# Kernel tuning notes

Hardware: AMD Instinct MI355X
Metric: run time of the kernel (lower is better)

## Reference

```python
import jax, jax.numpy as jnp
import numpy as np

B, L, D = 8, 1024, 512
H, DK, DV = 8, 64, 64
EPS = 1e-6
NEG = -1e9


def setup_inputs() -> dict:
    key = jax.random.key(0)
    ks = jax.random.split(key, 12)
    def xavier(k, shape):
        fan_out, fan_in = shape
        bound = float(np.sqrt(6.0 / (fan_in + fan_out)))
        return jax.random.uniform(k, shape, jnp.float32, -bound, bound)
    return {
        "q": jax.random.normal(ks[0], (B, L, D), jnp.float32),
        "k": jax.random.normal(ks[1], (B, L, D), jnp.float32),
        "v": jax.random.normal(ks[2], (B, L, D), jnp.float32),
        "event_type": jax.random.randint(ks[3], (B, L), 0, 2, jnp.int32),
        "mask": jax.random.randint(ks[4], (B, L, L), 0, 2, jnp.int32).astype(bool),
        "w_qs": xavier(ks[5], (H * DK, D)),
        "w_ex_en_qs": xavier(ks[6], (H * DK, D)),
        "w_ks": xavier(ks[7], (H * DK, D)),
        "w_vs": xavier(ks[8], (H * DV, D)),
        "w_fc": xavier(ks[9], (D, H * DV)),
        "b_fc": jnp.zeros((D,), jnp.float32),
        "ln_gamma": jnp.ones((D,), jnp.float32),
        "ln_beta": jnp.zeros((D,), jnp.float32),
    }


def _layer_norm(x, gamma, beta):
    mu = jnp.mean(x, axis=-1, keepdims=True)
    var = jnp.var(x, axis=-1, keepdims=True)
    return (x - mu) * jax.lax.rsqrt(var + EPS) * gamma + beta


def reference(q, k, v, event_type, mask, w_qs, w_ex_en_qs, w_ks, w_vs, w_fc, b_fc, ln_gamma, ln_beta):
    residual = q
    qn = _layer_norm(q, ln_gamma, ln_beta)  # normalize_before=True

    # event-type flags: en_en = prev is en AND present is en; ex_en = prev is ex AND present is en
    is_en = event_type != 0                                   # [B, L]
    en_en = (is_en[:, :, None] & is_en[:, None, :])[:, None]  # [B, 1, L, L]
    ex_en = ((~is_en)[:, :, None] & is_en[:, None, :])[:, None]

    def proj(x, w, d):  # torch Linear: x @ w.T, then split heads -> [B, H, L, d]
        return (x @ w.T).reshape(B, L, H, d).transpose(0, 2, 1, 3)

    q_en = proj(qn, w_qs, DK)
    q_ex = proj(qn, w_ex_en_qs, DK)
    kh = proj(k, w_ks, DK)
    vh = proj(v, w_vs, DV)

    temp = jnp.asarray(DK ** 0.5, qn.dtype)
    scores_en = jnp.einsum('bhqd,bhkd->bhqk', q_en / temp, kh)
    scores_en = jnp.where(mask[:, None], NEG, scores_en)      # masked branch
    scores_ex = jnp.einsum('bhqd,bhkd->bhqk', q_ex / temp, kh)  # unmasked branch

    blended = en_en * scores_en + ex_en * scores_ex           # [B, H, L, L]
    attn = jax.nn.softmax(blended, axis=-1)

    out = jnp.einsum('bhqk,bhkd->bhqd', attn, vh)             # PV
    out = out.transpose(0, 2, 1, 3).reshape(B, L, H * DV)
    out = out @ w_fc.T + b_fc
    out = out + residual
    return out, attn
```

## Files before the change

### kernel.cpp

```cpp
#include <hip/hip_runtime.h>

typedef __attribute__((ext_vector_type(8))) short bf16x8;
typedef __attribute__((ext_vector_type(4))) float f32x4;

#define DEVI static __device__ __forceinline__

constexpr float NEGV = -1e9f;

DEVI unsigned short f2b(float f) {
  union { float f; unsigned int u; } c; c.f = f;
  unsigned int lsb = (c.u >> 16) & 1u;
  return (unsigned short)((c.u + 0x7fffu + lsb) >> 16);
}
DEVI float sb2f(short s) {
  union { unsigned int u; float f; } c;
  c.u = ((unsigned int)(unsigned short)s) << 16;
  return c.f;
}

__global__ void mask_detect(const unsigned int* __restrict__ m, int n, int* flag) {
  unsigned int v = 0;
  for (int i = blockIdx.x * blockDim.x + threadIdx.x; i < n; i += gridDim.x * blockDim.x)
    v |= m[i];
  if (v & ~1u) atomicOr(flag, 1);
}

__global__ void mask_canon_bits(const void* __restrict__ mraw, unsigned int* __restrict__ mb,
                                int nwords, const int* __restrict__ flag) {
  int i = blockIdx.x * blockDim.x + threadIdx.x;
  if (i >= nwords) return;
  bool isbytes = (*flag != 0);
  unsigned int out = 0;
  if (isbytes) {
    const unsigned int* p = (const unsigned int*)mraw + (size_t)i * 8;
    #pragma unroll
    for (int w = 0; w < 8; w++) {
      unsigned int bw = p[w];
      out |= ((bw & 1u) << (w * 4)) | (((bw >> 8) & 1u) << (w * 4 + 1)) |
             (((bw >> 16) & 1u) << (w * 4 + 2)) | (((bw >> 24) & 1u) << (w * 4 + 3));
    }
  } else {
    const int4* p = (const int4*)mraw + (size_t)i * 8;
    #pragma unroll
    for (int w = 0; w < 8; w++) {
      int4 v = p[w];
      out |= ((v.x != 0 ? 1u : 0u) << (w * 4)) | ((v.y != 0 ? 1u : 0u) << (w * 4 + 1)) |
             ((v.z != 0 ? 1u : 0u) << (w * 4 + 2)) | ((v.w != 0 ? 1u : 0u) << (w * 4 + 3));
    }
  }
  mb[i] = out;
}

__global__ __launch_bounds__(256) void ln_kernel(const float* __restrict__ q,
    const float* __restrict__ gamma, const float* __restrict__ beta,
    unsigned short* __restrict__ qn) {
  int row = blockIdx.x;
  int t = threadIdx.x;
  const float* x = q + (size_t)row * 512;
  float2 v = reinterpret_cast<const float2*>(x)[t];
  float s = v.x + v.y, s2 = v.x * v.x + v.y * v.y;
  #pragma unroll
  for (int o = 32; o; o >>= 1) { s += __shfl_xor(s, o); s2 += __shfl_xor(s2, o); }
  __shared__ float ls[4], ls2[4];
  int w = t >> 6;
  if ((t & 63) == 0) { ls[w] = s; ls2[w] = s2; }
  __syncthreads();
  float S = ls[0] + ls[1] + ls[2] + ls[3];
  float S2 = ls2[0] + ls2[1] + ls2[2] + ls2[3];
  float mu = S * (1.f / 512.f);
  float var = S2 * (1.f / 512.f) - mu * mu;
  float r = rsqrtf(var + 1e-6f);
  float g0 = gamma[t * 2], g1 = gamma[t * 2 + 1];
  float b0 = beta[t * 2], b1 = beta[t * 2 + 1];
  ushort2 o;
  o.x = f2b((v.x - mu) * r * g0 + b0);
  o.y = f2b((v.y - mu) * r * g1 + b1);
  reinterpret_cast<ushort2*>(qn + (size_t)row * 512)[t] = o;
}

template<int MODE, bool CVX, bool CVW>
__global__ __launch_bounds__(256) void gemm_bt(
    const void* __restrict__ Xv,
    const void* __restrict__ Wv,
    void* __restrict__ Yv,
    float scale,
    const float* __restrict__ bias,
    const float* __restrict__ resid) {
  constexpr int LDT = 40;
  __shared__ __align__(16) unsigned short lA[64 * LDT];
  __shared__ __align__(16) unsigned short lB[64 * LDT];
  int t = threadIdx.x;
  int w = t >> 6, l = t & 63, lr = l & 15, lg = l >> 4;
  int mb = blockIdx.x * 64, nb = blockIdx.y * 64;
  f32x4 acc[4];
  #pragma unroll
  for (int n = 0; n < 4; n++) acc[n] = {0.f, 0.f, 0.f, 0.f};
  int sr = t >> 2, sc = (t & 3) * 8;
  for (int k0 = 0; k0 < 512; k0 += 32) {
    __syncthreads();
    if constexpr (CVX) {
      const float* src = (const float*)Xv + (size_t)(mb + sr) * 512 + k0 + sc;
      float4 x0 = *reinterpret_cast<const float4*>(src);
      float4 x1 = *reinterpret_cast<const float4*>(src + 4);
      ushort4 h0{f2b(x0.x), f2b(x0.y), f2b(x0.z), f2b(x0.w)};
      ushort4 h1{f2b(x1.x), f2b(x1.y), f2b(x1.z), f2b(x1.w)};
      *reinterpret_cast<ushort4*>(&lA[sr * LDT + sc]) = h0;
      *reinterpret_cast<ushort4*>(&lA[sr * LDT + sc + 4]) = h1;
    } else {
      *reinterpret_cast<float4*>(&lA[sr * LDT + sc]) =
          *reinterpret_cast<const float4*>((const unsigned short*)Xv + (size_t)(mb + sr) * 512 + k0 + sc);
    }
    if constexpr (CVW) {
      const float* src = (const float*)Wv + (size_t)(nb + sr) * 512 + k0 + sc;
      float4 x0 = *reinterpret_cast<const float4*>(src);
      float4 x1 = *reinterpret_cast<const float4*>(src + 4);
      ushort4 h0{f2b(x0.x), f2b(x0.y), f2b(x0.z), f2b(x0.w)};
      ushort4 h1{f2b(x1.x), f2b(x1.y), f2b(x1.z), f2b(x1.w)};
      *reinterpret_cast<ushort4*>(&lB[sr * LDT + sc]) = h0;
      *reinterpret_cast<ushort4*>(&lB[sr * LDT + sc + 4]) = h1;
    } else {
      *reinterpret_cast<float4*>(&lB[sr * LDT + sc]) =
          *reinterpret_cast<const float4*>((const unsigned short*)Wv + (size_t)(nb + sr) * 512 + k0 + sc);
    }
    __syncthreads();
    bf16x8 a = *reinterpret_cast<const bf16x8*>(&lA[(w * 16 + lr) * LDT + lg * 8]);
    #pragma unroll
    for (int n = 0; n < 4; n++) {
      bf16x8 bb = *reinterpret_cast<const bf16x8*>(&lB[(n * 16 + lr) * LDT + lg * 8]);
      acc[n] = __builtin_amdgcn_mfma_f32_16x16x32_bf16(a, bb, acc[n], 0, 0, 0);
    }
  }
  #pragma unroll
  for (int n = 0; n < 4; n++) {
    #pragma unroll
    for (int j = 0; j < 4; j++) {
      int m = mb + w * 16 + lg * 4 + j;
      int c = nb + n * 16 + lr;
      float val = acc[n][j] * scale;
      if constexpr (MODE == 0) {
        reinterpret_cast<unsigned short*>(Yv)[(size_t)m * 512 + c] = f2b(val);
      } else if constexpr (MODE == 1) {
        int bb_ = m >> 10, ll = m & 1023, hh = c >> 6, dd = c & 63;
        reinterpret_cast<unsigned short*>(Yv)[((size_t)((bb_ * 8 + hh) * 64 + dd)) * 1024 + ll] = f2b(val);
      } else {
        reinterpret_cast<float*>(Yv)[(size_t)m * 512 + c] =
            val + bias[c] + resid[(size_t)m * 512 + c];
      }
    }
  }
}

__global__ __launch_bounds__(256) void attn_kernel(
    const unsigned short* __restrict__ qen,
    const unsigned short* __restrict__ qex,
    const unsigned short* __restrict__ kh,
    const unsigned short* __restrict__ vhT,
    const int* __restrict__ etype,
    const unsigned int* __restrict__ mbits,
    float* __restrict__ attn_g,
    unsigned short* __restrict__ pv_out) {
  int lid = blockIdx.x;
  int xcd = lid & 7, slot = lid >> 3;
  int qt = slot & 15;
  int g = ((slot >> 4) << 3) | xcd;
  int h = g & 7, b = g >> 3;

  int t = threadIdx.x, w = t >> 6, l = t & 63, lr = l & 15, lg = l >> 4;
  __shared__ unsigned int ekbits[32];
  __shared__ unsigned int mkill[64 * 33];
  __shared__ __align__(16) unsigned short pbuf[4][16][40];

  int qb = qt * 64 + w * 16;
  int qrowA = qb + lr;
  bool evA = etype[b * 1024 + qrowA] != 0;
  const unsigned short* qp = evA ? qen : qex;
  size_t qoff = (size_t)(b * 1024 + qrowA) * 512 + h * 64;
  bf16x8 a0 = *reinterpret_cast<const bf16x8*>(qp + qoff + lg * 8);
  bf16x8 a1 = *reinterpret_cast<const bf16x8*>(qp + qoff + 32 + lg * 8);

  if (t < 32) {
    unsigned int wdd = 0;
    const int4* ep = (const int4*)(etype + b * 1024 + t * 32);
    #pragma unroll
    for (int j4 = 0; j4 < 8; j4++) {
      int4 e = ep[j4];
      wdd |= ((e.x != 0 ? 1u : 0u) << (j4 * 4)) | ((e.y != 0 ? 1u : 0u) << (j4 * 4 + 1)) |
             ((e.z != 0 ? 1u : 0u) << (j4 * 4 + 2)) | ((e.w != 0 ? 1u : 0u) << (j4 * 4 + 3));
    }
    ekbits[t] = wdd;
  }
  {
    const unsigned int* mslice = mbits + ((size_t)(b * 1024 + qt * 64)) * 32;
    for (int i = t; i < 2048; i += 256) {
      int row = i >> 5, wd = i & 31;
      bool evq_row = etype[b * 1024 + qt * 64 + row] != 0;
      mkill[row * 33 + wd] = evq_row ? mslice[i] : 0u;
    }
  }
  __syncthreads();

  int qrc[4], qlc[4];
  #pragma unroll
  for (int j = 0; j < 4; j++) { qlc[j] = w * 16 + lg * 4 + j; qrc[j] = qt * 64 + qlc[j]; }

  const unsigned short* kptr = kh + ((size_t)b * 1024 + lr) * 512 + h * 64 + lg * 8;
  const unsigned short* vptr = vhT + ((size_t)((b * 8 + h) * 64) + lr) * 1024 + lg * 8;

  float srun[4] = {0.f, 0.f, 0.f, 0.f};
  #pragma unroll 4
  for (int kt = 0; kt < 64; kt++) {
    const unsigned short* kp = kptr + (size_t)kt * 16 * 512;
    bf16x8 b0 = *reinterpret_cast<const bf16x8*>(kp);
    bf16x8 b1 = *reinterpret_cast<const bf16x8*>(kp + 32);
    f32x4 cc = {0.f, 0.f, 0.f, 0.f};
    cc = __builtin_amdgcn_mfma_f32_16x16x32_bf16(a0, b0, cc, 0, 0, 0);
    cc = __builtin_amdgcn_mfma_f32_16x16x32_bf16(a1, b1, cc, 0, 0, 0);
    int wcol = kt >> 1, bitpos = ((kt & 1) << 4) + lr;
    bool ekb = (ekbits[wcol] >> bitpos) & 1;
    #pragma unroll
    for (int j = 0; j < 4; j++) {
      bool mk = (mkill[qlc[j] * 33 + wcol] >> bitpos) & 1;
      float val = ekb ? (mk ? NEGV : cc[j]) : 0.f;
      srun[j] += __expf(val);
    }
  }
  float rS[4];
  #pragma unroll
  for (int j = 0; j < 4; j++) {
    float s = srun[j];
    s += __shfl_xor(s, 1); s += __shfl_xor(s, 2);
    s += __shfl_xor(s, 4); s += __shfl_xor(s, 8);
    rS[j] = 1.f / s;
  }

  f32x4 oacc[4];
  #pragma unroll
  for (int n = 0; n < 4; n++) oacc[n] = {0.f, 0.f, 0.f, 0.f};
  float* ag = attn_g + ((size_t)(b * 8 + h)) * 1024 * 1024;
  float* agrow = ag + (size_t)(qb + lr) * 1024 + lg * 8;

  #pragma unroll 2
  for (int kt = 0; kt < 64; kt++) {
    const unsigned short* kp = kptr + (size_t)kt * 16 * 512;
    bf16x8 b0 = *reinterpret_cast<const bf16x8*>(kp);
    bf16x8 b1 = *reinterpret_cast<const bf16x8*>(kp + 32);
    f32x4 cc = {0.f, 0.f, 0.f, 0.f};
    cc = __builtin_amdgcn_mfma_f32_16x16x32_bf16(a0, b0, cc, 0, 0, 0);
    cc = __builtin_amdgcn_mfma_f32_16x16x32_bf16(a1, b1, cc, 0, 0, 0);
    int wcol = kt >> 1, bitpos = ((kt & 1) << 4) + lr;
    bool ekb = (ekbits[wcol] >> bitpos) & 1;
    #pragma unroll
    for (int j = 0; j < 4; j++) {
      bool mk = (mkill[qlc[j] * 33 + wcol] >> bitpos) & 1;
      float val = ekb ? (mk ? NEGV : cc[j]) : 0.f;
      float p = __expf(val) * rS[j];
      pbuf[w][lg * 4 + j][((kt & 1) << 4) + lr] = f2b(p);
    }
    if (kt & 1) {
      int kc = kt >> 1;
      bf16x8 pa = *reinterpret_cast<const bf16x8*>(&pbuf[w][lr][lg * 8]);
      f32x4 f0, f1;
      f0[0] = sb2f(pa[0]); f0[1] = sb2f(pa[1]); f0[2] = sb2f(pa[2]); f0[3] = sb2f(pa[3]);
      f1[0] = sb2f(pa[4]); f1[1] = sb2f(pa[5]); f1[2] = sb2f(pa[6]); f1[3] = sb2f(pa[7]);
      __builtin_nontemporal_store(f0, reinterpret_cast<f32x4*>(agrow + kc * 32));
      __builtin_nontemporal_store(f1, reinterpret_cast<f32x4*>(agrow + kc * 32 + 4));
      #pragma unroll
      for (int n = 0; n < 4; n++) {
        const unsigned short* vp = vptr + (size_t)n * 16 * 1024 + kc * 32;
        bf16x8 vb = *reinterpret_cast<const bf16x8*>(vp);
        oacc[n] = __builtin_amdgcn_mfma_f32_16x16x32_bf16(pa, vb, oacc[n], 0, 0, 0);
      }
    }
  }
  #pragma unroll
  for (int n = 0; n < 4; n++) {
    #pragma unroll
    for (int j = 0; j < 4; j++) {
      __builtin_nontemporal_store(f2b(oacc[n][j]),
          &pv_out[(size_t)(b * 1024 + qrc[j]) * 512 + h * 64 + n * 16 + lr]);
    }
  }
}

extern "C" void kernel_launch(void* const* d_in, const int* in_sizes, int n_in,
                              void* d_out, int out_size, void* d_ws, size_t ws_size,
                              hipStream_t stream) {
  (void)in_sizes; (void)n_in; (void)out_size; (void)ws_size;
  const float* q     = (const float*)d_in[0];
  const float* k     = (const float*)d_in[1];
  const float* v     = (const float*)d_in[2];
  const int* etype   = (const int*)d_in[3];
  const void* mask_raw = d_in[4];
  const float* w_qs  = (const float*)d_in[5];
  const float* w_ex  = (const float*)d_in[6];
  const float* w_ks  = (const float*)d_in[7];
  const float* w_vs  = (const float*)d_in[8];
  const float* w_fc  = (const float*)d_in[9];
  const float* b_fc  = (const float*)d_in[10];
  const float* gamma = (const float*)d_in[11];
  const float* beta  = (const float*)d_in[12];

  char* ws = (char*)d_ws;
  const size_t MB = 1024 * 1024;
  unsigned short* qn   = (unsigned short*)(ws);
  unsigned short* qen  = (unsigned short*)(ws + 8 * MB);
  unsigned short* qex  = (unsigned short*)(ws + 16 * MB);
  unsigned short* khb  = (unsigned short*)(ws + 24 * MB);
  unsigned short* vhT  = (unsigned short*)(ws + 32 * MB);
  unsigned short* ao   = (unsigned short*)(ws + 40 * MB);
  unsigned int* mbits  = (unsigned int*)(ws + 48 * MB);
  int* mflag           = (int*)(ws + 49 * MB);

  float* outp = (float*)d_out;
  float* attn_g = outp + (size_t)8 * 1024 * 512;

  ln_kernel<<<8192, 256, 0, stream>>>(q, gamma, beta, qn);

  const int MASK_N = 8 * 1024 * 1024;
  hipMemsetAsync(mflag, 0, 4, stream);
  mask_detect<<<2048, 256, 0, stream>>>((const unsigned int*)mask_raw, MASK_N / 4, mflag);
  const int NWORDS = MASK_N / 32;
  mask_canon_bits<<<(NWORDS + 255) / 256, 256, 0, stream>>>(mask_raw, mbits, NWORDS, mflag);

  dim3 gg(128, 8);
  gemm_bt<0, false, true><<<gg, 256, 0, stream>>>(qn, w_qs, qen, 0.125f, nullptr, nullptr);
  gemm_bt<0, false, true><<<gg, 256, 0, stream>>>(qn, w_ex, qex, 0.125f, nullptr, nullptr);
  gemm_bt<0, true,  true><<<gg, 256, 0, stream>>>(k,  w_ks, khb, 1.0f, nullptr, nullptr);
  gemm_bt<1, true,  true><<<gg, 256, 0, stream>>>(v,  w_vs, vhT, 1.0f, nullptr, nullptr);

  attn_kernel<<<dim3(1024), 256, 0, stream>>>(qen, qex, khb, vhT, etype, mbits,
                                              attn_g, ao);

  gemm_bt<2, false, true><<<gg, 256, 0, stream>>>(ao, w_fc, outp, 1.0f, b_fc, q);
}
```

Baseline: 318.0 us.

## Split attention key range across two wave groups per block

The attention block grows from 4 to 8 waves. Each group of four waves handles half of the key columns for the same 64 query rows. The partial softmax sums from the two groups are combined through shared memory. The partial PV accumulators are reduced through an LDS buffer before the output is written. The aim is more in-flight waves per CU to hide the latency of the global K/V loads and of the large attention-matrix stores. The cost is extra barriers, more LDS (about 17KB for oshare), and launch bounds that may limit registers.

```diff
diff --git a/kernel.cpp b/kernel.cpp
--- a/kernel.cpp
+++ b/kernel.cpp
@@ -150,7 +150,7 @@
   }
 }
 
-__global__ __launch_bounds__(256) void attn_kernel(
+__global__ __launch_bounds__(512, 8) void attn_kernel(
     const unsigned short* __restrict__ qen,
     const unsigned short* __restrict__ qex,
     const unsigned short* __restrict__ kh,
@@ -166,11 +166,15 @@
   int h = g & 7, b = g >> 3;
 
   int t = threadIdx.x, w = t >> 6, l = t & 63, lr = l & 15, lg = l >> 4;
+  int rowgrp = w & 3, khalf = w >> 2;
+
   __shared__ unsigned int ekbits[32];
   __shared__ unsigned int mkill[64 * 33];
-  __shared__ __align__(16) unsigned short pbuf[4][16][40];
-
-  int qb = qt * 64 + w * 16;
+  __shared__ __align__(16) unsigned short pbuf[8][16][40];
+  __shared__ float sred[2][64];
+  __shared__ __align__(16) float oshare[64][65];
+
+  int qb = qt * 64 + rowgrp * 16;
   int qrowA = qb + lr;
   bool evA = etype[b * 1024 + qrowA] != 0;
   const unsigned short* qp = evA ? qen : qex;
@@ -185,13 +189,13 @@
     for (int j4 = 0; j4 < 8; j4++) {
       int4 e = ep[j4];
       wdd |= ((e.x != 0 ? 1u : 0u) << (j4 * 4)) | ((e.y != 0 ? 1u : 0u) << (j4 * 4 + 1)) |
-             ((e.z != 0 ? 1u : 0u) << (j4 * 4 + 2)) | ((e.w != 0 ? 1u : 0u) << (j4 * 4 + 3));
+             (((e.z != 0 ? 1u : 0u)) << (j4 * 4 + 2)) | ((e.w != 0 ? 1u : 0u) << (j4 * 4 + 3));
     }
     ekbits[t] = wdd;
   }
   {
     const unsigned int* mslice = mbits + ((size_t)(b * 1024 + qt * 64)) * 32;
-    for (int i = t; i < 2048; i += 256) {
+    for (int i = t; i < 2048; i += 512) {
       int row = i >> 5, wd = i & 31;
       bool evq_row = etype[b * 1024 + qt * 64 + row] != 0;
       mkill[row * 33 + wd] = evq_row ? mslice[i] : 0u;
@@ -201,21 +205,21 @@
 
   int qrc[4], qlc[4];
   #pragma unroll
-  for (int j = 0; j < 4; j++) { qlc[j] = w * 16 + lg * 4 + j; qrc[j] = qt * 64 + qlc[j]; }
-
-  const unsigned short* kptr = kh + ((size_t)b * 1024 + lr) * 512 + h * 64 + lg * 8;
-  const unsigned short* vptr = vhT + ((size_t)((b * 8 + h) * 64) + lr) * 1024 + lg * 8;
+  for (int j = 0; j < 4; j++) { qlc[j] = rowgrp * 16 + lg * 4 + j; qrc[j] = qt * 64 + qlc[j]; }
+
+  const unsigned short* kptr = kh + ((size_t)b * 1024 + khalf * 512 + lr) * 512 + h * 64 + lg * 8;
+  const unsigned short* vptr = vhT + ((size_t)((b * 8 + h) * 64) + lr) * 1024 + khalf * 512 + lg * 8;
 
   float srun[4] = {0.f, 0.f, 0.f, 0.f};
   #pragma unroll 4
-  for (int kt = 0; kt < 64; kt++) {
-    const unsigned short* kp = kptr + (size_t)kt * 16 * 512;
+  for (int kt2 = 0; kt2 < 32; kt2++) {
+    const unsigned short* kp = kptr + (size_t)kt2 * 16 * 512;
     bf16x8 b0 = *reinterpret_cast<const bf16x8*>(kp);
     bf16x8 b1 = *reinterpret_cast<const bf16x8*>(kp + 32);
     f32x4 cc = {0.f, 0.f, 0.f, 0.f};
     cc = __builtin_amdgcn_mfma_f32_16x16x32_bf16(a0, b0, cc, 0, 0, 0);
     cc = __builtin_amdgcn_mfma_f32_16x16x32_bf16(a1, b1, cc, 0, 0, 0);
-    int wcol = kt >> 1, bitpos = ((kt & 1) << 4) + lr;
+    int wcol = khalf * 16 + (kt2 >> 1), bitpos = ((kt2 & 1) << 4) + lr;
     bool ekb = (ekbits[wcol] >> bitpos) & 1;
     #pragma unroll
     for (int j = 0; j < 4; j++) {
@@ -224,40 +228,43 @@
       srun[j] += __expf(val);
     }
   }
-  float rS[4];
   #pragma unroll
   for (int j = 0; j < 4; j++) {
     float s = srun[j];
     s += __shfl_xor(s, 1); s += __shfl_xor(s, 2);
     s += __shfl_xor(s, 4); s += __shfl_xor(s, 8);
-    rS[j] = 1.f / s;
-  }
+    if (lr == 0) sred[khalf][qlc[j]] = s;
+  }
+  __syncthreads();
+  float rS[4];
+  #pragma unroll
+  for (int j = 0; j < 4; j++) rS[j] = 1.f / (sred[0][qlc[j]] + sred[1][qlc[j]]);
 
   f32x4 oacc[4];
   #pragma unroll
   for (int n = 0; n < 4; n++) oacc[n] = {0.f, 0.f, 0.f, 0.f};
   float* ag = attn_g + ((size_t)(b * 8 + h)) * 1024 * 1024;
-  float* agrow = ag + (size_t)(qb + lr) * 1024 + lg * 8;
+  float* agrow = ag + (size_t)(qb + lr) * 1024 + khalf * 512 + lg * 8;
 
   #pragma unroll 2
-  for (int kt = 0; kt < 64; kt++) {
-    const unsigned short* kp = kptr + (size_t)kt * 16 * 512;
+  for (int kt2 = 0; kt2 < 32; kt2++) {
+    const unsigned short* kp = kptr + (size_t)kt2 * 16 * 512;
     bf16x8 b0 = *reinterpret_cast<const bf16x8*>(kp);
     bf16x8 b1 = *reinterpret_cast<const bf16x8*>(kp + 32);
     f32x4 cc = {0.f, 0.f, 0.f, 0.f};
     cc = __builtin_amdgcn_mfma_f32_16x16x32_bf16(a0, b0, cc, 0, 0, 0);
     cc = __builtin_amdgcn_mfma_f32_16x16x32_bf16(a1, b1, cc, 0, 0, 0);
-    int wcol = kt >> 1, bitpos = ((kt & 1) << 4) + lr;
+    int wcol = khalf * 16 + (kt2 >> 1), bitpos = ((kt2 & 1) << 4) + lr;
     bool ekb = (ekbits[wcol] >> bitpos) & 1;
     #pragma unroll
     for (int j = 0; j < 4; j++) {
       bool mk = (mkill[qlc[j] * 33 + wcol] >> bitpos) & 1;
       float val = ekb ? (mk ? NEGV : cc[j]) : 0.f;
       float p = __expf(val) * rS[j];
-      pbuf[w][lg * 4 + j][((kt & 1) << 4) + lr] = f2b(p);
-    }
-    if (kt & 1) {
-      int kc = kt >> 1;
+      pbuf[w][lg * 4 + j][((kt2 & 1) << 4) + lr] = f2b(p);
+    }
+    if (kt2 & 1) {
+      int kc = kt2 >> 1;
       bf16x8 pa = *reinterpret_cast<const bf16x8*>(&pbuf[w][lr][lg * 8]);
       f32x4 f0, f1;
       f0[0] = sb2f(pa[0]); f0[1] = sb2f(pa[1]); f0[2] = sb2f(pa[2]); f0[3] = sb2f(pa[3]);
@@ -272,12 +279,24 @@
       }
     }
   }
-  #pragma unroll
-  for (int n = 0; n < 4; n++) {
-    #pragma unroll
-    for (int j = 0; j < 4; j++) {
-      __builtin_nontemporal_store(f2b(oacc[n][j]),
-          &pv_out[(size_t)(b * 1024 + qrc[j]) * 512 + h * 64 + n * 16 + lr]);
+
+  if (khalf == 0) {
+    #pragma unroll
+    for (int n = 0; n < 4; n++)
+      #pragma unroll
+      for (int j = 0; j < 4; j++)
+        oshare[qlc[j]][n * 16 + lr] = oacc[n][j];
+  }
+  __syncthreads();
+  if (khalf == 1) {
+    #pragma unroll
+    for (int n = 0; n < 4; n++) {
+      #pragma unroll
+      for (int j = 0; j < 4; j++) {
+        float v = oacc[n][j] + oshare[qlc[j]][n * 16 + lr];
+        __builtin_nontemporal_store(f2b(v),
+            &pv_out[(size_t)(b * 1024 + qrc[j]) * 512 + h * 64 + n * 16 + lr]);
+      }
     }
   }
 }
@@ -328,7 +347,7 @@
   gemm_bt<0, true,  true><<<gg, 256, 0, stream>>>(k,  w_ks, khb, 1.0f, nullptr, nullptr);
   gemm_bt<1, true,  true><<<gg, 256, 0, stream>>>(v,  w_vs, vhT, 1.0f, nullptr, nullptr);
 
-  attn_kernel<<<dim3(1024), 256, 0, stream>>>(qen, qex, khb, vhT, etype, mbits,
+  attn_kernel<<<dim3(1024), 512, 0, stream>>>(qen, qex, khb, vhT, etype, mbits,
                                               attn_g, ao);
 
   gemm_bt<2, false, true><<<gg, 256, 0, stream>>>(ao, w_fc, outp, 1.0f, b_fc, q);
```

Result: faster. 300.1 us (-5.6%).
